# Kernel tuning notes

Measured on AMD Instinct MI355X. Metric: run time of the kernel, lower is better.

## Reference

```python
import jax, jax.numpy as jnp
import numpy as np

LEAK = 0.2

def leaky(x):
    return jnp.where(x > 0, x, LEAK * x)

def relu(x):
    return jnp.maximum(x, 0)

def conv1d(x, w):
    # x [B,Cin,L], w [Cout,Cin,3], stride 1, padding 1
    return jax.lax.conv_general_dilated(x, w, (1,), [(1, 1)],
        dimension_numbers=('NCH', 'OIH', 'NCH'))

def conv2d(x, w, pad, dil=1, groups=1):
    return jax.lax.conv_general_dilated(x, w, (1, 1), [(pad, pad), (pad, pad)],
        rhs_dilation=(dil, dil), feature_group_count=groups,
        dimension_numbers=('NCHW', 'OIHW', 'NCHW'))

def bn2d(x, p, eps=1e-5):
    # p: [4,C] = gamma, beta, running_mean, running_var (eval-mode BN)
    g, b, m, v = p
    s = (1, -1, 1, 1)
    return (x - m.reshape(s)) * (g.reshape(s) / jnp.sqrt(v.reshape(s) + eps)) + b.reshape(s)

def layernorm(x, g, b, eps=1e-5):
    mu = x.mean(-1, keepdims=True)
    var = ((x - mu) ** 2).mean(-1, keepdims=True)
    return (x - mu) / jnp.sqrt(var + eps) * g + b

def l2n(x, axis, eps):
    n = jnp.sqrt((x * x).sum(axis, keepdims=True))
    return x / jnp.maximum(n, eps)


def setup_inputs() -> dict:
    key = jax.random.key(0)
    B, C, H, W = 4, 64, 48, 48
    D, Fn, T, V = 256, 8, 4, 16
    E = 16  # orthogonal prototype embed dim
    ks = iter(jax.random.split(key, 64))
    def rn(shape, s=0.05):
        return jax.random.normal(next(ks), shape, jnp.float32) * s
    def bnp(c):
        return jnp.stack([1.0 + rn((c,), 0.1), rn((c,), 0.1), rn((c,), 0.1), 1.0 + jnp.abs(rn((c,), 0.1))])
    return dict(
        basis_vector_bank=jax.random.normal(next(ks), (T, V, D), jnp.float32),
        task_f=jax.random.normal(next(ks), (B, C, 16, 16), jnp.float32),
        img_f=jax.random.normal(next(ks), (B, C, H, W), jnp.float32),
        protos=jax.random.normal(next(ks), (T, E), jnp.float32),
        tA_w1=rn((E // 4, 1, 3)), tA_w2=rn((E // 2, E // 4, 3)),
        iA_w=rn((E // 2, C, 3, 3)), iA_bn=bnp(E // 2),
        at_w1=rn((E, Fn // 2 * E)), at_b1=rn((Fn // 2 * E,)),
        at_ln_g=jnp.ones((Fn // 2 * E,)), at_ln_b=jnp.zeros((Fn // 2 * E,)),
        at_w2=rn((Fn // 2 * E, Fn * E)), at_b2=rn((Fn * E,)),
        bv_t1=rn((D // 4, 1, 3)), bv_t2=rn((D // 2, D // 4, 3)),
        bv_ic1=rn((D // 4, C, 3, 3)), bv_bn1=bnp(D // 4),
        bv_ic2=rn((D // 2, D // 4, 3, 3)), bv_bn2=bnp(D // 2),
        bv_w1=rn((D, D // 4)), bv_b1=rn((D // 4,)),
        bv_ln_g=jnp.ones((D // 4,)), bv_ln_b=jnp.zeros((D // 4,)),
        bv_w2=rn((D // 4, D)), bv_b2=rn((D,)),
        m1_w1=rn((D, D // 4)), m1_b1=rn((D // 4,)),
        m1_ln_g=jnp.ones((D // 4,)), m1_ln_b=jnp.zeros((D // 4,)),
        m1_w2=rn((D // 4, C * C)), m1_b2=rn((C * C,)),
        m3_w1=rn((D, D // 4)), m3_b1=rn((D // 4,)),
        m3_ln_g=jnp.ones((D // 4,)), m3_ln_b=jnp.zeros((D // 4,)),
        m3_w2=rn((D // 4, 9 * C * C)), m3_b2=rn((9 * C * C,)),
        blr_bn=bnp(C),
        zc_w=rn((C, C, 1, 1), 0.01), zc_b=rn((C,), 0.01),
    )


def _forward(basis_vector_bank, task_f, img_f, protos, tA_w1, tA_w2, iA_w, iA_bn,
             at_w1, at_b1, at_ln_g, at_ln_b, at_w2, at_b2,
             bv_t1, bv_t2, bv_ic1, bv_bn1, bv_ic2, bv_bn2,
             bv_w1, bv_b1, bv_ln_g, bv_ln_b, bv_w2, bv_b2,
             m1_w1, m1_b1, m1_ln_g, m1_ln_b, m1_w2, m1_b2,
             m3_w1, m3_b1, m3_ln_g, m3_ln_b, m3_w2, m3_b2,
             blr_bn, zc_w, zc_b):
    T, V, D = basis_vector_bank.shape
    B, C, H, W = img_f.shape
    E = protos.shape[1]
    Fn = at_w2.shape[1] // E
    tau = 0.5

    # --- A2SI routing features ---
    xt = task_f.reshape(B, 1, -1)
    t1 = conv1d(leaky(conv1d(xt, tA_w1)), tA_w2).mean(-1)          # [B,E/2]
    i1 = leaky(bn2d(conv2d(img_f, iA_w, 1), iA_bn)).mean((2, 3))   # [B,E/2]
    f1 = jnp.concatenate([t1, i1], axis=1)                         # [B,E]
    h = relu(layernorm(f1 @ at_w1 + at_b1, at_ln_g, at_ln_b))
    tif = (h @ at_w2 + at_b2).reshape(B, E, Fn)                    # [B,E,F]
    logits = jnp.einsum('te,bef->bft', l2n(protos, -1, 1e-8), l2n(tif, 1, 1e-8))  # [B,F,T]

    # hard gumbel-softmax (straight-through), fixed noise key for determinism
    u = jax.random.uniform(jax.random.key(42), logits.shape, jnp.float32, 1e-10, 1.0)
    g = -jnp.log(-jnp.log(u))
    y = jax.nn.softmax((logits + g) / tau, axis=-1)
    idx = jnp.argmax(y, axis=-1)                                   # [B,F]
    y_hard = jax.nn.one_hot(idx, T, dtype=y.dtype)
    set_type = y_hard + y - jax.lax.stop_gradient(y)

    bank_flat = basis_vector_bank.reshape(T, V * D)
    sbvb = jnp.einsum('bft,tk->bfk', set_type, bank_flat).reshape(B, Fn, V, D)

    # --- BasisV_filter: filter feature ---
    xt2 = task_f.reshape(B, C, -1)
    rms = jnp.sqrt((xt2 ** 2).mean((1, 2), keepdims=True))
    xt2 = (xt2 / (rms + 1e-8)).reshape(B, 1, -1)
    te = conv1d(leaky(conv1d(xt2, bv_t1)), bv_t2).mean(-1)         # [B,D/2]
    ie = leaky(bn2d(conv2d(img_f, bv_ic1, 1), bv_bn1))
    ie = leaky(bn2d(conv2d(ie, bv_ic2, 1), bv_bn2)).mean((2, 3))   # [B,D/2]
    ff = jnp.concatenate([te, ie], axis=1)                         # [B,D]
    ff = relu(layernorm(ff @ bv_w1 + bv_b1, bv_ln_g, bv_ln_b)) @ bv_w2 + bv_b2

    # --- per-(batch,type) group gather/top-k/scatter, vectorized ---
    # group bank = bank of first filter with that type (hard one-hot -> type's bank)
    occ = idx[:, None, :] == jnp.arange(T)[None, :, None]          # [B,T,F]
    first = jnp.argmax(occ, axis=-1)                               # [B,T]
    Bg = jnp.take_along_axis(sbvb, first[:, :, None, None], axis=1)  # [B,T,V,D]
    # all rows of Q within a group are identical (filter_f expanded over F),
    # so S.max(0) == cosine(ff[b], Bg[b,t])
    scores = jnp.einsum('bd,btvd->btv', l2n(ff, -1, 1e-12), l2n(Bg, -1, 1e-12))
    order = jnp.argsort(-scores, axis=-1)                          # [B,T,V] topk order
    lt = jnp.tril(jnp.ones((Fn, Fn), bool), -1)                    # j < i
    rank = ((idx[:, :, None] == idx[:, None, :]) & lt).sum(-1)     # position in group
    bidx = jnp.arange(B)[:, None]
    sel = order[bidx, idx, rank]                                   # [B,F]
    bvf = Bg[bidx, idx, sel]                                       # [B,F,D]

    # --- per-filter dynamic convolutions ---
    w1 = relu(layernorm(bvf @ m1_w1 + m1_b1, m1_ln_g, m1_ln_b)) @ m1_w2 + m1_b2
    w1 = w1.reshape(B, Fn, C, C)                                   # [B,F,out,in]
    w3 = relu(layernorm(bvf @ m3_w1 + m3_b1, m3_ln_g, m3_ln_b)) @ m3_w2 + m3_b2
    w3 = w3.reshape(B * Fn, C, C, 3, 3)

    dp0 = jnp.einsum('bfoc,bchw->bfohw', w1, img_f)                # 1x1 branch
    xin = jnp.broadcast_to(img_f[:, None], (B, Fn, C, H, W)).reshape(1, B * Fn * C, H, W)
    ker = w3.reshape(B * Fn * C, C, 3, 3)
    dpd = [conv2d(xin, ker, d, dil=d, groups=B * Fn).reshape(B, Fn, C, H, W)
           for d in (1, 2, 3)]                                     # same-padded dilated 3x3
    t_ = idx[:, :, None, None, None]
    dp = jnp.where(t_ == 0, dp0, jnp.where(t_ == 1, dpd[0],
         jnp.where(t_ == 2, dpd[1], dpd[2])))                      # [B,F,C,H,W]

    x = leaky(bn2d(dp.reshape(B * Fn, C, H, W), blr_bn)).reshape(B, Fn, C, H, W).mean(1)
    a = conv2d(x, zc_w, 0) + zc_b.reshape(1, -1, 1, 1)
    return a + img_f


@jax.jit
def reference(basis_vector_bank, task_f, img_f, protos, tA_w1, tA_w2, iA_w, iA_bn,
              at_w1, at_b1, at_ln_g, at_ln_b, at_w2, at_b2,
              bv_t1, bv_t2, bv_ic1, bv_bn1, bv_ic2, bv_bn2,
              bv_w1, bv_b1, bv_ln_g, bv_ln_b, bv_w2, bv_b2,
              m1_w1, m1_b1, m1_ln_g, m1_ln_b, m1_w2, m1_b2,
              m3_w1, m3_b1, m3_ln_g, m3_ln_b, m3_w2, m3_b2,
              blr_bn, zc_w, zc_b):
    return _forward(basis_vector_bank, task_f, img_f, protos, tA_w1, tA_w2, iA_w, iA_bn,
                    at_w1, at_b1, at_ln_g, at_ln_b, at_w2, at_b2,
                    bv_t1, bv_t2, bv_ic1, bv_bn1, bv_ic2, bv_bn2,
                    bv_w1, bv_b1, bv_ln_g, bv_ln_b, bv_w2, bv_b2,
                    m1_w1, m1_b1, m1_ln_g, m1_ln_b, m1_w2, m1_b2,
                    m3_w1, m3_b1, m3_ln_g, m3_ln_b, m3_w2, m3_b2,
                    blr_bn, zc_w, zc_b)
```

## Files before the change

kernel.cpp:

```cpp
#include <hip/hip_runtime.h>
#include <math.h>

#define LEAKC 0.2f

#define NB 4
#define NC 64
#define LLEN 16384
#define HW 2304
#define PP 54
#define PHW 2916
#define SLABP 72
#define CP 72
#define IE1C 50

typedef __attribute__((ext_vector_type(8))) short short8;
typedef __attribute__((ext_vector_type(4))) float floatx4;

__device__ __forceinline__ float leaky(float x){ return x > 0.f ? x : LEAKC*x; }

__device__ __forceinline__ float wave_sum64(float v){
  for(int off=32;off;off>>=1) v += __shfl_xor(v,off);
  return v;
}

__device__ __forceinline__ unsigned short f2bf(float x){
  unsigned u=__float_as_uint(x);
  unsigned r=u+0x7FFFu+((u>>16)&1u);
  return (unsigned short)(r>>16);
}

__device__ __forceinline__ void threefry2x32(unsigned k0, unsigned k1, unsigned& x0, unsigned& x1){
  unsigned ks0=k0, ks1=k1, ks2=k0^k1^0x1BD11BDAu;
  x0+=ks0; x1+=ks1;
  const int rot0[4]={13,15,26,6};
  const int rot1[4]={17,29,16,24};
#define TF_APPLY(rr) {for(int r=0;r<4;r++){x0+=x1; x1=(x1<<rr[r])|(x1>>(32-rr[r])); x1^=x0;}}
  TF_APPLY(rot0); x0+=ks1; x1+=ks2+1u;
  TF_APPLY(rot1); x0+=ks2; x1+=ks0+2u;
  TF_APPLY(rot0); x0+=ks0; x1+=ks1+3u;
  TF_APPLY(rot1); x0+=ks1; x1+=ks2+4u;
  TF_APPLY(rot0); x0+=ks2; x1+=ks0+5u;
#undef TF_APPLY
}

__device__ __forceinline__ float jax_uniform128(int i){
  unsigned x0=0u, x1=(unsigned)i;
  threefry2x32(0u,42u,x0,x1);
  unsigned bits = x0 ^ x1;
  unsigned fb=(bits>>9)|0x3f800000u;
  float f=__uint_as_float(fb)-1.0f;
  float u=f*(1.0f-1e-10f)+1e-10f;
  return fmaxf(1e-10f,u);
}

struct MidSM {
  float sT[64], s0[64], sL[64];
  float red8[64][9];
  float totA_s[4]; float rms_s;
  float part[512];
  float te_s[128], t1_s[8];
  float f1[16], h[64], tif[128], tifn[128], tden[8], pden[4], pn[64], z[32];
  int sidx[8], sfirst[4], srank[8], rows[8];
  float iered[128];
  float fbuf[256], hh[64], ffn_s[256], finv_s;
  float scores[64];
  int order[64];
  float bvf[2048];
};

__global__ __launch_bounds__(256) void k_pre(const float* __restrict__ task_f,
                      const float* __restrict__ w1A, const float* __restrict__ w1B,
                      float* __restrict__ totApart, float* __restrict__ a0A, float* __restrict__ aLA,
                      float* __restrict__ totBpart, float* __restrict__ a0B, float* __restrict__ aLB,
                      float* __restrict__ rmspart,
                      const float* __restrict__ img,
                      const float* __restrict__ w1, const float* __restrict__ w2,
                      const float* __restrict__ wa,
                      unsigned short* __restrict__ imgTP,
                      unsigned short* __restrict__ W1T, unsigned short* __restrict__ W2T,
                      unsigned short* __restrict__ WAT,
                      const float* __restrict__ mw1, const float* __restrict__ mw3,
                      const float* __restrict__ bvw1p, const float* __restrict__ bvw2p,
                      const float* __restrict__ bvt2p, const float* __restrict__ atw2p,
                      const float* __restrict__ bankp,
                      const float* __restrict__ m1w2p, const float* __restrict__ m3w2p,
                      const float* __restrict__ zcwp,
                      float* __restrict__ warm, int* __restrict__ donec){
  if(blockIdx.x<256){
    int b=blockIdx.x>>6, seg=blockIdx.x&63;
    const float* x=task_f+b*LLEN;
    float tA[4]={0,0,0,0};
    float tB[64];
#pragma unroll
    for(int c=0;c<64;c++) tB[c]=0.f;
    float sq=0.f;
    int l=seg*256+threadIdx.x;
    {
      float xm=(l>0)?x[l-1]:0.f;
      float xc=x[l];
      float xp=(l<LLEN-1)?x[l+1]:0.f;
      sq=xc*xc;
#pragma unroll
      for(int c=0;c<4;c++){
        float a=leaky(w1A[c*3+0]*xm + w1A[c*3+1]*xc + w1A[c*3+2]*xp);
        tA[c]=a;
        if(l==0) a0A[b*4+c]=a;
        if(l==LLEN-1) aLA[b*4+c]=a;
      }
#pragma unroll
      for(int c=0;c<64;c++){
        float a=leaky(w1B[c*3+0]*xm + w1B[c*3+1]*xc + w1B[c*3+2]*xp);
        tB[c]=a;
        if(l==0) a0B[b*64+c]=a;
        if(l==LLEN-1) aLB[b*64+c]=a;
      }
    }
    sq=wave_sum64(sq);
#pragma unroll
    for(int c=0;c<4;c++) tA[c]=wave_sum64(tA[c]);
#pragma unroll
    for(int c=0;c<64;c++){
      float v=tB[c];
      for(int off=32;off;off>>=1) v+=__shfl_down(v,off);
      tB[c]=v;
    }
    __shared__ float redB[4][64];
    __shared__ float redA[4][4];
    __shared__ float redQ[4];
    int wave=threadIdx.x>>6, lane=threadIdx.x&63;
    if(lane==0){
#pragma unroll
      for(int c=0;c<64;c++) redB[wave][c]=tB[c];
#pragma unroll
      for(int c=0;c<4;c++) redA[wave][c]=tA[c];
      redQ[wave]=sq;
    }
    __syncthreads();
    if(threadIdx.x<64){
      float s=redB[0][threadIdx.x]+redB[1][threadIdx.x]+redB[2][threadIdx.x]+redB[3][threadIdx.x];
      totBpart[(size_t)(b*64+seg)*64+threadIdx.x]=s;
    } else if(threadIdx.x<68){
      int c=threadIdx.x-64;
      totApart[(b*64+seg)*4+c]=redA[0][c]+redA[1][c]+redA[2][c]+redA[3][c];
    } else if(threadIdx.x==68){
      rmspart[b*64+seg]=redQ[0]+redQ[1]+redQ[2]+redQ[3];
    }
  } else if(blockIdx.x<400){
    int blk=blockIdx.x-256;
    int b=blk/36, t=blk%36;
    int p0=t*64;
    __shared__ float tile[64][65];
    int pp=threadIdx.x&63, c4=threadIdx.x>>6;
    for(int r=0;r<16;r++){
      int c=c4*16+r;
      tile[c][pp]=img[(b*64+c)*HW + p0+pp];
    }
    __syncthreads();
    int pxl=threadIdx.x>>2, cg=(threadIdx.x&3)*16;
    unsigned out[8];
#pragma unroll
    for(int q=0;q<8;q++){
      unsigned lo=f2bf(tile[cg+2*q][pxl]);
      unsigned hi=f2bf(tile[cg+2*q+1][pxl]);
      out[q]=lo|(hi<<16);
    }
    int px=p0+pxl;
    int h=px/48, w=px-h*48;
    int poff=(h+3)*PP+(w+3);
    unsigned* dst=(unsigned*)(imgTP + ((size_t)(b*PHW+poff))*64 + cg);
#pragma unroll
    for(int q=0;q<8;q++) dst[q]=out[q];
  } else if(blockIdx.x<868){
    int n=(blockIdx.x-400)*256+threadIdx.x;
    if(n<9*64*64){
      int tap=n>>12, oc=(n>>6)&63, c=n&63;
      W1T[n]=f2bf(w1[oc*576+c*9+tap]);
    } else if(n<9*64*64+9*128*64){
      int m=n-9*64*64;
      int tap=m/8192, r=m-tap*8192, oc=r>>6, c=r&63;
      W2T[m]=f2bf(w2[oc*576+c*9+tap]);
    } else {
      int q=n-9*64*64-9*128*64;
      if(q<9*16*64){
        int tap=q>>10, r=q&1023, o=r>>6, c=r&63;
        WAT[q]=(o<8)?f2bf(wa[o*576+c*9+tap]):(unsigned short)0;
      }
    }
  } else if(blockIdx.x<932){
    int t=(blockIdx.x-868)*256+threadIdx.x;
    float a=0.f;
    for(int i=t;i*16<16384;i+=16384) a+=mw1[i*16];
    for(int i=t;i*16<16384;i+=16384) a+=mw3[i*16];
    for(int i=t;i*16<16384;i+=16384) a+=bvw1p[i*16];
    for(int i=t;i*16<16384;i+=16384) a+=bvw2p[i*16];
    for(int i=t;i*16<24576;i+=16384) a+=bvt2p[i*16];
    for(int i=t;i*16<8192;i+=16384) a+=atw2p[i*16];
    for(int i=t;i*16<16384;i+=16384) a+=bankp[i*16];
    for(int i=t;i*16<262144;i+=16384) a+=m1w2p[i*16];
    for(int i=t;i*16<2359296;i+=16384) a+=m3w2p[i*16];
    for(int i=t;i*16<4096;i+=16384) a+=zcwp[i*16];
    warm[t&1023]=a;
  } else {
    if(blockIdx.x==932 && threadIdx.x==0) *donec=0;
    int id=(blockIdx.x-932)*256+threadIdx.x;
    uint4 z=make_uint4(0,0,0,0);
    for(int cch=id;cch<19584;cch+=4096){
      int ck=cch&7, pxid=cch>>3;
      int b=pxid/612, p=pxid-b*612;
      int h,w;
      if(p<324){ int r=p/54; w=p-r*54; h=(r<3)?r:(r+48); }
      else { int q=p-324; int r2=q/6; int cc=q-r2*6; h=3+r2; w=(cc<3)?cc:(cc+48); }
      *(uint4*)(imgTP + ((size_t)(b*PHW + h*PP + w))*64 + ck*8)=z;
    }
  }
}

__global__ __launch_bounds__(512) void k_cm(const unsigned short* __restrict__ imgTP,
    const unsigned short* __restrict__ W1T, const unsigned short* __restrict__ W2T,
    const unsigned short* __restrict__ WAT,
    const float* __restrict__ bn1, const float* __restrict__ bn2, const float* __restrict__ bnA,
    float* __restrict__ iepart, float* __restrict__ i1part,
    const float* __restrict__ totApart, const float* __restrict__ a0A, const float* __restrict__ aLA,
    const float* __restrict__ totBpart, const float* __restrict__ a0B, const float* __restrict__ aLB,
    const float* __restrict__ rmspart,
    const float* __restrict__ tA_w2, const float* __restrict__ bv_t2,
    const float* __restrict__ at_w1, const float* __restrict__ at_b1,
    const float* __restrict__ at_ln_g, const float* __restrict__ at_ln_b,
    const float* __restrict__ at_w2, const float* __restrict__ at_b2,
    const float* __restrict__ protos,
    const float* __restrict__ bv_w1, const float* __restrict__ bv_b1,
    const float* __restrict__ bv_ln_g, const float* __restrict__ bv_ln_b,
    const float* __restrict__ bv_w2, const float* __restrict__ bv_b2,
    const float* __restrict__ bank,
    const float* __restrict__ m1_w1, const float* __restrict__ m1_b1,
    const float* __restrict__ m1_g,  const float* __restrict__ m1_bb,
    const float* __restrict__ m3_w1, const float* __restrict__ m3_b1,
    const float* __restrict__ m3_g,  const float* __restrict__ m3_bb,
    int* __restrict__ idxo, float* __restrict__ hid1, float* __restrict__ hid3,
    int* __restrict__ donec){
  __shared__ __align__(16) char smraw[75456];
  int tid=threadIdx.x;
  int lane=tid&63, wv=tid>>6;
  int n0=lane&15, kg=lane>>4;
  if(blockIdx.x<96){
    int blk=blockIdx.x;
    int b=blk/24, hp=blk-b*24;
    int h0=hp*2;
    unsigned short* slab=(unsigned short*)smraw;
    unsigned short* ie1=(unsigned short*)(smraw+46656);
    {
      const unsigned short* ibase=imgTP+((size_t)b*PHW+(size_t)(h0+1)*PP)*64;
      for(int e=tid;e<6*54*8;e+=512){
        int rr=e/(54*8), rem=e-rr*54*8, w=rem>>3, ck=rem&7;
        uint4 v=*(const uint4*)(ibase+((size_t)(rr*PP+w))*64+ck*8);
        *(uint4*)(slab+(rr*54+w)*SLABP+ck*8)=v;
      }
      if(tid<64){
        int br=tid>>4, cq=(tid>>3)&1, ck=tid&7;
        *(uint4*)(ie1+((size_t)(br*IE1C+(cq?49:0)))*CP+ck*8)=make_uint4(0,0,0,0);
      }
    }
    __syncthreads();
    {
      int mt=wv&3, rh=wv>>2;
      floatx4 acc[2][3];
#pragma unroll
      for(int rr=0;rr<2;rr++)
#pragma unroll
        for(int nt=0;nt<3;nt++) acc[rr][nt]=(floatx4){0.f,0.f,0.f,0.f};
#pragma unroll
      for(int ti=0;ti<3;ti++){
#pragma unroll
        for(int tj=0;tj<3;tj++){
          int tap=ti*3+tj;
          const unsigned short* Ab=W1T+(size_t)tap*4096;
#pragma unroll
          for(int c0=0;c0<64;c0+=32){
            short8 a=*(const short8*)(Ab+((mt*16+n0)*64+c0+kg*8));
#pragma unroll
            for(int rr=0;rr<2;rr++){
              int sr=rh*2+rr+ti;
#pragma unroll
              for(int nt=0;nt<3;nt++){
                int sc=nt*16+n0+tj+2;
                short8 bv=*(const short8*)(slab+(sr*54+sc)*SLABP+c0+kg*8);
                acc[rr][nt]=__builtin_amdgcn_mfma_f32_16x16x32_bf16(a,bv,acc[rr][nt],0,0,0);
              }
            }
          }
        }
      }
      int obase=mt*16+kg*4;
      float scale[4],m_[4],be_[4];
#pragma unroll
      for(int reg=0;reg<4;reg++){
        int o=obase+reg;
        scale[reg]=bn1[o]/sqrtf(bn1[192+o]+1e-5f);
        m_[reg]=bn1[128+o]; be_[reg]=bn1[64+o];
      }
#pragma unroll
      for(int rr=0;rr<2;rr++){
        int br=rh*2+rr;
        bool rv=((unsigned)(h0-1+br))<48u;
#pragma unroll
        for(int nt=0;nt<3;nt++){
          float v0=rv?leaky((acc[rr][nt][0]-m_[0])*scale[0]+be_[0]):0.f;
          float v1=rv?leaky((acc[rr][nt][1]-m_[1])*scale[1]+be_[1]):0.f;
          float v2=rv?leaky((acc[rr][nt][2]-m_[2])*scale[2]+be_[2]):0.f;
          float v3=rv?leaky((acc[rr][nt][3]-m_[3])*scale[3]+be_[3]):0.f;
          unsigned w0=f2bf(v0)|((unsigned)f2bf(v1)<<16);
          unsigned w1=f2bf(v2)|((unsigned)f2bf(v3)<<16);
          uint2 pk={w0,w1};
          *(uint2*)(ie1+((size_t)(br*IE1C+(nt*16+1+n0)))*CP+obase)=pk;
        }
      }
    }
    __syncthreads();
    {
      int mt2=wv;
      floatx4 acc[6];
#pragma unroll
      for(int i=0;i<6;i++) acc[i]=(floatx4){0.f,0.f,0.f,0.f};
#pragma unroll
      for(int ti=0;ti<3;ti++){
#pragma unroll
        for(int tj=0;tj<3;tj++){
          int tap=ti*3+tj;
          const unsigned short* Ab=W2T+(size_t)tap*8192;
#pragma unroll
          for(int c0=0;c0<64;c0+=32){
            short8 a=*(const short8*)(Ab+((mt2*16+n0)*64+c0+kg*8));
#pragma unroll
            for(int rr=0;rr<2;rr++){
              int sr=rr+ti;
#pragma unroll
              for(int wc=0;wc<3;wc++){
                int q=wc*16+n0+tj;
                short8 bv=*(const short8*)(ie1+((size_t)(sr*IE1C+q))*CP+c0+kg*8);
                acc[rr*3+wc]=__builtin_amdgcn_mfma_f32_16x16x32_bf16(a,bv,acc[rr*3+wc],0,0,0);
              }
            }
          }
        }
      }
      int obase=mt2*16+kg*4;
#pragma unroll
      for(int reg=0;reg<4;reg++){
        int o=obase+reg;
        float scale=bn2[o]/sqrtf(bn2[384+o]+1e-5f);
        float m_=bn2[256+o], be_=bn2[128+o];
        float part=0;
#pragma unroll
        for(int i=0;i<6;i++) part+=leaky((acc[i][reg]-m_)*scale+be_);
        for(int off=1;off<16;off<<=1) part+=__shfl_xor(part,off);
        if(n0==0) iepart[(b*24+hp)*128+o]=part*(1.f/2304.f);
      }
    }
    __syncthreads();
    if(tid==0) __hip_atomic_fetch_add(donec,1,__ATOMIC_RELEASE,__HIP_MEMORY_SCOPE_AGENT);
  } else if(blockIdx.x<108){
    int blk2=blockIdx.x-96;
    int b=blk2/3, hg=blk2%3;
    int hp=hg*8+wv;
    int h0=hp*2;
    const unsigned short* ib=imgTP+(size_t)b*PHW*64;
    floatx4 acc[6];
#pragma unroll
    for(int i=0;i<6;i++) acc[i]=(floatx4){0.f,0.f,0.f,0.f};
#pragma unroll
    for(int ti=0;ti<3;ti++){
#pragma unroll
      for(int tj=0;tj<3;tj++){
        int tap=ti*3+tj;
        const unsigned short* Ab=WAT+(size_t)tap*1024;
#pragma unroll
        for(int c0=0;c0<64;c0+=32){
          short8 a=*(const short8*)(Ab+(n0*64+c0+kg*8));
#pragma unroll
          for(int rr=0;rr<2;rr++){
            int r=h0+rr+ti-1+3;
#pragma unroll
            for(int wc=0;wc<3;wc++){
              int w=wc*16+n0+tj-1+3;
              short8 bv=*(const short8*)(ib+((size_t)(r*PP+w)*64+c0+kg*8));
              acc[rr*3+wc]=__builtin_amdgcn_mfma_f32_16x16x32_bf16(a,bv,acc[rr*3+wc],0,0,0);
            }
          }
        }
      }
    }
    int obase=kg*4;
#pragma unroll
    for(int reg=0;reg<4;reg++){
      int o=obase+reg;
      float part=0;
      if(o<8){
        float scale=bnA[o]/sqrtf(bnA[24+o]+1e-5f);
        float m_=bnA[16+o], be_=bnA[8+o];
#pragma unroll
        for(int i=0;i<6;i++) part+=leaky((acc[i][reg]-m_)*scale+be_);
      }
      for(int off=1;off<16;off<<=1) part+=__shfl_xor(part,off);
      if(n0==0 && o<8) i1part[(b*24+hp)*8+o]=part*(1.f/2304.f);
    }
    __syncthreads();
    if(tid==0) __hip_atomic_fetch_add(donec,1,__ATOMIC_RELEASE,__HIP_MEMORY_SCOPE_AGENT);
  } else {
    MidSM* S=(MidSM*)smraw;
    int b=blockIdx.x-108;
    const float invL=1.0f/16384.0f;
    {
      int c8=tid>>3, g8=tid&7;
      float s8=0;
#pragma unroll
      for(int seg=g8*8;seg<g8*8+8;seg++) s8+=totBpart[(size_t)(b*64+seg)*64+c8];
      S->red8[c8][g8]=s8;
    }
    if(tid>=64 && tid<128){
      int t=tid-64;
      S->s0[t]=a0B[b*64+t]; S->sL[t]=aLB[b*64+t];
    } else if(tid>=128 && tid<192){
      float v=rmspart[b*64+(tid-128)];
      v=wave_sum64(v);
      if(tid==128) S->rms_s=v;
    } else if(tid>=192 && tid<196){
      int c=tid-192;
      float s=0;
#pragma unroll 8
      for(int seg=0;seg<64;seg++) s+=totApart[(b*64+seg)*4+c];
      S->totA_s[c]=s;
    }
    __syncthreads();
    if(tid<64){
      float s=0;
#pragma unroll
      for(int g=0;g<8;g++) s+=S->red8[tid][g];
      S->sT[tid]=s;
    }
    __syncthreads();
    float scB=1.0f/(sqrtf(S->rms_s*invL)+1e-8f);
    if(tid<256){
      int c2=tid&127, h2=tid>>7;
      const float* wr=bv_t2+c2*192;
      float s=0;
      for(int c1=h2*32;c1<h2*32+32;c1+=8){
        float4 q[6];
        const float4* r4=(const float4*)(wr+c1*3);
#pragma unroll
        for(int u=0;u<6;u++) q[u]=r4[u];
        const float* qq=(const float*)q;
#pragma unroll
        for(int u=0;u<8;u++){
          int c=c1+u;
          float T=S->sT[c], A0=S->s0[c], AL=S->sL[c];
          s += qq[u*3+0]*(T-AL) + qq[u*3+1]*T + qq[u*3+2]*(T-A0);
        }
      }
      S->part[tid]=s;
    } else if(tid>=384 && tid<392){
      int c2=tid-384;
      float s=0;
      for(int c1=0;c1<4;c1++){
        float T=S->totA_s[c1], A0=a0A[b*4+c1], AL=aLA[b*4+c1];
        const float* w=&tA_w2[(c2*4+c1)*3];
        s += w[0]*(T-AL) + w[1]*T + w[2]*(T-A0);
      }
      S->t1_s[c2]=s*invL;
    }
    __syncthreads();
    if(tid<128) S->te_s[tid]=(S->part[tid]+S->part[tid+128])*invL*scB;
    __syncthreads();
    if(tid==0){
      while(__hip_atomic_load(donec,__ATOMIC_ACQUIRE,__HIP_MEMORY_SCOPE_AGENT)<108)
        __builtin_amdgcn_s_sleep(8);
    }
    __syncthreads();
    if(tid<8) S->f1[tid]=S->t1_s[tid];
    else if(tid<16){
      int f=tid-8;
      float s=0;
#pragma unroll
      for(int g=0;g<24;g++) s+=i1part[(b*24+g)*8+f];
      S->f1[tid]=s;
    } else if(tid>=256 && tid<384){
      int c=tid-256;
      float s=0;
#pragma unroll 8
      for(int g=0;g<24;g++) s+=iepart[(b*24+g)*128+c];
      S->iered[c]=s;
    }
    __syncthreads();
    if(tid<64){
      float s=at_b1[lane];
#pragma unroll
      for(int i=0;i<16;i++) s+=S->f1[i]*at_w1[i*64+lane];
      float mu=wave_sum64(s)*(1.f/64.f);
      float d=s-mu;
      float var=wave_sum64(d*d)*(1.f/64.f);
      S->h[lane]=fmaxf(d*(1.0f/sqrtf(var+1e-5f))*at_ln_g[lane]+at_ln_b[lane],0.f);
    }
    __syncthreads();
    if(tid<256){
      int n=tid&127, h2=tid>>7;
      float a0=0,a1=0;
      for(int k=h2*32;k<h2*32+32;k+=2){
        a0+=S->h[k]*at_w2[k*128+n];
        a1+=S->h[k+1]*at_w2[(k+1)*128+n];
      }
      S->part[tid]=a0+a1;
    }
    __syncthreads();
    if(tid<128) S->tif[tid]=at_b2[tid]+S->part[tid]+S->part[tid+128];
    __syncthreads();
    if(tid<8){
      int f=tid;
      float ss=0; for(int e=0;e<16;e++){float v=S->tif[e*8+f]; ss+=v*v;}
      S->tden[f]=fmaxf(sqrtf(ss),1e-8f);
    } else if(tid<12){
      int t=tid-8;
      float ss=0; for(int e=0;e<16;e++){float v=protos[t*16+e]; ss+=v*v;}
      S->pden[t]=fmaxf(sqrtf(ss),1e-8f);
    }
    __syncthreads();
    if(tid<128) S->tifn[tid]=S->tif[tid]/S->tden[tid&7];
    if(tid<64) S->pn[tid]=protos[tid]/S->pden[tid>>4];
    __syncthreads();
    if(tid<32){
      int f=tid>>2, t=tid&3;
      float ss=0;
#pragma unroll
      for(int e=0;e<16;e++) ss+=S->pn[t*16+e]*S->tifn[e*8+f];
      float u=jax_uniform128(b*32+f*4+t);
      float g=-logf(-logf(u));
      S->z[tid]=ss+g;
    }
    __syncthreads();
    if(tid<8){
      float best=S->z[tid*4]; int bi=0;
      for(int t=1;t<4;t++){ float v=S->z[tid*4+t]; if(v>best){best=v;bi=t;} }
      S->sidx[tid]=bi;
    }
    __syncthreads();
    if(tid<4){
      int t=tid;
      int fi=0;
      for(int f=7;f>=0;f--) if(S->sidx[f]==t) fi=f;
      S->sfirst[t]=fi;
    } else if(tid<12){
      int f=tid-4;
      int c=0; for(int f2=0;f2<f;f2++) if(S->sidx[f2]==S->sidx[f]) c++;
      S->srank[f]=c;
    }
    __syncthreads();

    if(tid<128) S->fbuf[tid]=S->te_s[tid];
    else if(tid<256) S->fbuf[tid]=S->iered[tid-128];
    __syncthreads();
    if(tid<256){
      int l64=tid&63, q=tid>>6;
      float a0=0,a1=0,a2=0,a3=0;
      for(int k=q*64;k<q*64+64;k+=4){
        a0+=S->fbuf[k]  *bv_w1[k*64+l64];
        a1+=S->fbuf[k+1]*bv_w1[(k+1)*64+l64];
        a2+=S->fbuf[k+2]*bv_w1[(k+2)*64+l64];
        a3+=S->fbuf[k+3]*bv_w1[(k+3)*64+l64];
      }
      S->part[tid]=((a0+a1)+(a2+a3));
    }
    __syncthreads();
    if(tid<64){
      float s=bv_b1[lane]+S->part[lane]+S->part[64+lane]+S->part[128+lane]+S->part[192+lane];
      float mu=wave_sum64(s)*(1.f/64.f);
      float d=s-mu;
      float var=wave_sum64(d*d)*(1.f/64.f);
      S->hh[lane]=fmaxf(d*(1.0f/sqrtf(var+1e-5f))*bv_ln_g[lane]+bv_ln_b[lane],0.f);
    }
    __syncthreads();
    {
      int n=tid&255, h2=tid>>8;
      float a0=0,a1=0;
      for(int k=h2*32;k<h2*32+32;k+=2){
        a0+=S->hh[k]*bv_w2[k*256+n];
        a1+=S->hh[k+1]*bv_w2[(k+1)*256+n];
      }
      S->part[tid]=a0+a1;
    }
    __syncthreads();
    if(tid<256) S->ffn_s[tid]=bv_b2[tid]+S->part[tid]+S->part[tid+256];
    __syncthreads();
    if(tid<64){
      float sq=0;
#pragma unroll
      for(int u=0;u<4;u++){ float v=S->ffn_s[u*64+lane]; sq+=v*v; }
      sq=wave_sum64(sq);
      if(lane==0) S->finv_s=1.0f/fmaxf(sqrtf(sq),1e-12f);
    }
    __syncthreads();
    if(tid<256) S->ffn_s[tid]*=S->finv_s;
    __syncthreads();

    if(tid<128){
      int it=tid&63, h2=tid>>6;
      int t=it>>4, v=it&15;
      int tt=S->sidx[S->sfirst[t]];
      const float4* row=(const float4*)(bank+(tt*16+v)*256);
      float sa=0,na=0;
      for(int d4=h2*32;d4<h2*32+32;d4++){
        float4 r=row[d4];
        const float* fp=&S->ffn_s[d4*4];
        sa+=fp[0]*r.x+fp[1]*r.y+fp[2]*r.z+fp[3]*r.w;
        na+=r.x*r.x+r.y*r.y+r.z*r.z+r.w*r.w;
      }
      S->part[tid]=sa;
      S->part[256+tid]=na;
    }
    __syncthreads();
    if(tid<64) S->scores[tid]=(S->part[tid]+S->part[tid+64])/fmaxf(sqrtf(S->part[256+tid]+S->part[320+tid]),1e-12f);
    __syncthreads();
    if(tid<4){
      const float* sc=&S->scores[tid*16];
      unsigned used=0;
      for(int pk=0;pk<16;pk++){
        int best=-1; float bv=-1e30f;
        for(int v2=0;v2<16;v2++){
          if(used&(1u<<v2)) continue;
          float vv=sc[v2];
          if(best<0||vv>bv){bv=vv;best=v2;}
        }
        used|=1u<<best;
        S->order[tid*16+pk]=best;
      }
    }
    __syncthreads();
    if(tid<8){
      int t=S->sidx[tid];
      int v=S->order[t*16+S->srank[tid]];
      S->rows[tid]=t*16+v;
      idxo[b*8+tid]=t;
    }
    __syncthreads();

    for(int ii=tid;ii<2048;ii+=512){
      int r=ii>>8, d=ii&255;
      S->bvf[ii]=bank[S->rows[r]*256+d];
    }
    __syncthreads();
    {
      int r=wv;
      const float* bp=&S->bvf[r*256];
      float a0=0,a1=0,a2=0,a3=0;
      float c0=0,c1=0,c2=0,c3=0;
      for(int d=0;d<256;d+=4){
        float b0=bp[d],b1=bp[d+1],b2=bp[d+2],b3=bp[d+3];
        a0+=b0*m1_w1[d*64+lane];
        a1+=b1*m1_w1[(d+1)*64+lane];
        a2+=b2*m1_w1[(d+2)*64+lane];
        a3+=b3*m1_w1[(d+3)*64+lane];
        c0+=b0*m3_w1[d*64+lane];
        c1+=b1*m3_w1[(d+1)*64+lane];
        c2+=b2*m3_w1[(d+2)*64+lane];
        c3+=b3*m3_w1[(d+3)*64+lane];
      }
      float s1=m1_b1[lane]+((a0+a1)+(a2+a3));
      float s3=m3_b1[lane]+((c0+c1)+(c2+c3));
      float mu=wave_sum64(s1)*(1.f/64.f);
      float dd=s1-mu;
      float var=wave_sum64(dd*dd)*(1.f/64.f);
      hid1[(b*8+r)*64+lane]=fmaxf(dd*(1.0f/sqrtf(var+1e-5f))*m1_g[lane]+m1_bb[lane],0.f);
      mu=wave_sum64(s3)*(1.f/64.f);
      dd=s3-mu;
      var=wave_sum64(dd*dd)*(1.f/64.f);
      hid3[(b*8+r)*64+lane]=fmaxf(dd*(1.0f/sqrtf(var+1e-5f))*m3_g[lane]+m3_bb[lane],0.f);
    }
  }
}

__global__ __launch_bounds__(256) void k_heads(const float* __restrict__ hid1, const float* __restrict__ hid3,
                        const float* __restrict__ w2a, const float* __restrict__ b2a,
                        const float* __restrict__ w2b, const float* __restrict__ b2b,
                        unsigned short* __restrict__ A1, unsigned short* __restrict__ A3){
  __shared__ float hl[2048];
  if(blockIdx.x<16){
    int n=blockIdx.x*256+threadIdx.x;
    float wcol[64];
#pragma unroll
    for(int k=0;k<64;k++) wcol[k]=w2a[k*4096+n];
    float bb=b2a[n];
    for(int i=threadIdx.x;i<2048;i+=256) hl[i]=hid1[i];
    __syncthreads();
    for(int bf=0;bf<32;bf++){
      float s=bb;
#pragma unroll
      for(int k=0;k<64;k++) s+=hl[bf*64+k]*wcol[k];
      A1[bf*4096+n]=f2bf(s);
    }
  } else {
    int n=(blockIdx.x-16)*256+threadIdx.x;
    float wcol[64];
#pragma unroll
    for(int k=0;k<64;k++) wcol[k]=w2b[(size_t)k*36864+n];
    float bb=b2b[n];
    for(int i=threadIdx.x;i<2048;i+=256) hl[i]=hid3[i];
    __syncthreads();
    int o=n/576, rem=n-o*576;
    int c=rem/9, tap=rem-c*9;
    size_t base=((size_t)tap*64+o)*64+c;
    for(int bf=0;bf<32;bf++){
      float s=bb;
#pragma unroll
      for(int k=0;k<64;k++) s+=hl[bf*64+k]*wcol[k];
      A3[(size_t)bf*9*4096+base]=f2bf(s);
    }
  }
}

__global__ __launch_bounds__(512) void k_dynF(const unsigned short* __restrict__ imgTP,
                       const unsigned short* __restrict__ A1, const unsigned short* __restrict__ A3,
                       const int* __restrict__ idx, const float* __restrict__ bn,
                       const float* __restrict__ zc_w, const float* __restrict__ zc_b,
                       const float* __restrict__ img, float* __restrict__ out){
  int blk=blockIdx.x;
  int b=blk/48, r0=blk-b*48;
  int tid=threadIdx.x;
  int lane=tid&63, w8=tid>>6;
  int mt=w8&3, fh=w8>>2;
  int n0=lane&15, kg=lane>>4;
  __shared__ unsigned short slab[7*54*SLABP];
  __shared__ float xl[64*50];
  __shared__ float zl[4096];
  int tts[4];
#pragma unroll
  for(int i=0;i<4;i++) tts[i]=idx[b*8+fh*4+i];
  int obase=mt*16+kg*4;
  float scale[4],m_[4],be_[4];
#pragma unroll
  for(int reg=0;reg<4;reg++){
    int o=obase+reg;
    scale[reg]=bn[o]/sqrtf(bn[192+o]+1e-5f);
    m_[reg]=bn[128+o]; be_[reg]=bn[64+o];
  }
  for(int i=tid;i<4096;i+=512) zl[i]=zc_w[i];
  for(int i=tid;i<3200;i+=512) xl[i]=0.f;
  {
    const unsigned short* ibase=imgTP+((size_t)b*PHW+(size_t)r0*PP)*64;
    for(int e=tid;e<7*54*8;e+=512){
      int rr=e/(54*8), rem=e-rr*54*8, w=rem>>3, ck=rem&7;
      uint4 v=*(const uint4*)(ibase + ((size_t)(rr*PP+w))*64 + ck*8);
      *(uint4*)(slab + (rr*54+w)*SLABP + ck*8)=v;
    }
  }
  __syncthreads();
  float xsum[3][4];
#pragma unroll
  for(int wc=0;wc<3;wc++)
#pragma unroll
    for(int reg=0;reg<4;reg++) xsum[wc][reg]=0.f;
#pragma unroll
  for(int fi=0;fi<4;fi++){
    int f=fh*4+fi;
    int bf=b*8+f;
    int tt=tts[fi];
    floatx4 acc[3];
#pragma unroll
    for(int i=0;i<3;i++) acc[i]=(floatx4){0.f,0.f,0.f,0.f};
    if(tt==0){
      const unsigned short* Ab=A1+(size_t)bf*4096;
#pragma unroll
      for(int c0=0;c0<64;c0+=32){
        short8 a=*(const short8*)(Ab+((mt*16+n0)*64+c0+kg*8));
#pragma unroll
        for(int wc=0;wc<3;wc++){
          short8 bv=*(const short8*)(slab + (3*54 + wc*16+n0+3)*SLABP + c0+kg*8);
          acc[wc]=__builtin_amdgcn_mfma_f32_16x16x32_bf16(a,bv,acc[wc],0,0,0);
        }
      }
    } else {
      int d=tt;
      const unsigned short* A3b=A3+(size_t)bf*9*4096;
#pragma unroll
      for(int ti=0;ti<3;ti++){
        int lr=d*(ti-1)+3;
#pragma unroll
        for(int tj=0;tj<3;tj++){
          int tap=ti*3+tj;
          int dw=d*(tj-1)+3;
          const unsigned short* Ab=A3b+(size_t)tap*4096;
#pragma unroll
          for(int c0=0;c0<64;c0+=32){
            short8 a=*(const short8*)(Ab+((mt*16+n0)*64+c0+kg*8));
#pragma unroll
            for(int wc=0;wc<3;wc++){
              short8 bv=*(const short8*)(slab + (lr*54 + wc*16+n0+dw)*SLABP + c0+kg*8);
              acc[wc]=__builtin_amdgcn_mfma_f32_16x16x32_bf16(a,bv,acc[wc],0,0,0);
            }
          }
        }
      }
    }
#pragma unroll
    for(int wc=0;wc<3;wc++)
#pragma unroll
      for(int reg=0;reg<4;reg++)
        xsum[wc][reg]+=leaky((acc[wc][reg]-m_[reg])*scale[reg]+be_[reg]);
  }
#pragma unroll
  for(int wc=0;wc<3;wc++)
#pragma unroll
    for(int reg=0;reg<4;reg++)
      atomicAdd(&xl[(obase+reg)*50 + wc*16+n0], xsum[wc][reg]*0.125f);
  __syncthreads();
  size_t base=(size_t)b*64*HW + r0*48;
  for(int e=tid;e<3072;e+=512){
    int o=e/48, px=e-o*48;
    float s=zc_b[o];
#pragma unroll
    for(int c=0;c<64;c++) s+=zl[o*64+c]*xl[c*50+px];
    size_t a=base+(size_t)o*HW+px;
    out[a]=s+img[a];
  }
}

extern "C" void kernel_launch(void* const* d_in, const int* in_sizes, int n_in,
                              void* d_out, int out_size, void* d_ws, size_t ws_size,
                              hipStream_t stream){
  const float* bank   =(const float*)d_in[0];
  const float* task_f =(const float*)d_in[1];
  const float* img_f  =(const float*)d_in[2];
  const float* protos =(const float*)d_in[3];
  const float* tA_w1  =(const float*)d_in[4];
  const float* tA_w2  =(const float*)d_in[5];
  const float* iA_w   =(const float*)d_in[6];
  const float* iA_bn  =(const float*)d_in[7];
  const float* at_w1  =(const float*)d_in[8];
  const float* at_b1  =(const float*)d_in[9];
  const float* at_ln_g=(const float*)d_in[10];
  const float* at_ln_b=(const float*)d_in[11];
  const float* at_w2  =(const float*)d_in[12];
  const float* at_b2  =(const float*)d_in[13];
  const float* bv_t1  =(const float*)d_in[14];
  const float* bv_t2  =(const float*)d_in[15];
  const float* bv_ic1 =(const float*)d_in[16];
  const float* bv_bn1 =(const float*)d_in[17];
  const float* bv_ic2 =(const float*)d_in[18];
  const float* bv_bn2 =(const float*)d_in[19];
  const float* bv_w1  =(const float*)d_in[20];
  const float* bv_b1  =(const float*)d_in[21];
  const float* bv_ln_g=(const float*)d_in[22];
  const float* bv_ln_b=(const float*)d_in[23];
  const float* bv_w2  =(const float*)d_in[24];
  const float* bv_b2  =(const float*)d_in[25];
  const float* m1_w1  =(const float*)d_in[26];
  const float* m1_b1  =(const float*)d_in[27];
  const float* m1_ln_g=(const float*)d_in[28];
  const float* m1_ln_b=(const float*)d_in[29];
  const float* m1_w2  =(const float*)d_in[30];
  const float* m1_b2  =(const float*)d_in[31];
  const float* m3_w1  =(const float*)d_in[32];
  const float* m3_b1  =(const float*)d_in[33];
  const float* m3_ln_g=(const float*)d_in[34];
  const float* m3_ln_b=(const float*)d_in[35];
  const float* m3_w2  =(const float*)d_in[36];
  const float* m3_b2  =(const float*)d_in[37];
  const float* blr_bn =(const float*)d_in[38];
  const float* zc_w   =(const float*)d_in[39];
  const float* zc_b   =(const float*)d_in[40];

  float* ws=(float*)d_ws;
  float* totApart=ws+0;
  float* a0A  =ws+1024;
  float* aLA  =ws+1040;
  float* totBpart=ws+1056;
  float* a0B  =ws+17440;
  float* aLB  =ws+17696;
  float* rmspart=ws+17952;
  float* i1part =ws+18208;
  float* iepart =ws+18976;
  int*   idxp   =(int*)(ws+31264);
  float* hid1=ws+31296;
  float* hid3=ws+33344;
  unsigned short* A1p  =(unsigned short*)(ws+35392);
  unsigned short* A3p  =(unsigned short*)(ws+100928);
  unsigned short* imgTP=(unsigned short*)(ws+690752);
  unsigned short* W1Tp =(unsigned short*)(ws+1064000);
  unsigned short* W2Tp =(unsigned short*)(ws+1082432);
  unsigned short* WATp =(unsigned short*)(ws+1119296);
  float* warm =ws+1123904;
  int*   donec=(int*)(ws+1124928);

  k_pre<<<948,256,0,stream>>>(task_f, tA_w1, bv_t1,
                              totApart, a0A, aLA, totBpart, a0B, aLB, rmspart,
                              img_f, bv_ic1, bv_ic2, iA_w, imgTP, W1Tp, W2Tp, WATp,
                              m1_w1, m3_w1, bv_w1, bv_w2, bv_t2, at_w2, bank,
                              m1_w2, m3_w2, zc_w, warm, donec);
  k_cm<<<112,512,0,stream>>>(imgTP, W1Tp, W2Tp, WATp, bv_bn1, bv_bn2, iA_bn,
                             iepart, i1part,
                             totApart, a0A, aLA, totBpart, a0B, aLB, rmspart,
                             tA_w2, bv_t2,
                             at_w1, at_b1, at_ln_g, at_ln_b, at_w2, at_b2, protos,
                             bv_w1, bv_b1, bv_ln_g, bv_ln_b, bv_w2, bv_b2, bank,
                             m1_w1, m1_b1, m1_ln_g, m1_ln_b,
                             m3_w1, m3_b1, m3_ln_g, m3_ln_b,
                             idxp, hid1, hid3, donec);
  k_heads<<<160,256,0,stream>>>(hid1, hid3, m1_w2, m1_b2, m3_w2, m3_b2, A1p, A3p);
  k_dynF<<<192,512,0,stream>>>(imgTP, A1p, A3p, idxp, blr_bn, zc_w, zc_b, img_f, (float*)d_out);

  (void)in_sizes; (void)n_in; (void)out_size; (void)ws_size;
}
```

Measured before the change: 266.1 us.

## Fuse head GEMMs and dynamic conv into one kernel with atomic-counter handoff

Merges the k_heads and k_dynF kernels into a single launch. The first 80 blocks compute the A1/A3 head weights and bump a global counter. The remaining 192 conv blocks stage their image slab, then spin until all producers are done. This removes one kernel launch and its boundary, and lets slab loading overlap with head computation. The cost is spin-waiting, and the scheme depends on all 272 blocks being co-resident. The zc weights now reuse the slab's shared memory after the MFMA phase.

```diff
diff --git a/kernel.cpp b/kernel.cpp
--- a/kernel.cpp
+++ b/kernel.cpp
@@ -61,7 +61,6 @@
   float te_s[128], t1_s[8];
   float f1[16], h[64], tif[128], tifn[128], tden[8], pden[4], pn[64], z[32];
   int sidx[8], sfirst[4], srank[8], rows[8];
-  float iered[128];
   float fbuf[256], hh[64], ffn_s[256], finv_s;
   float scores[64];
   int order[64];
@@ -85,7 +84,7 @@
                       const float* __restrict__ bankp,
                       const float* __restrict__ m1w2p, const float* __restrict__ m3w2p,
                       const float* __restrict__ zcwp,
-                      float* __restrict__ warm, int* __restrict__ donec){
+                      float* __restrict__ warm, int* __restrict__ cnt){
   if(blockIdx.x<256){
     int b=blockIdx.x>>6, seg=blockIdx.x&63;
     const float* x=task_f+b*LLEN;
@@ -201,7 +200,8 @@
     for(int i=t;i*16<4096;i+=16384) a+=zcwp[i*16];
     warm[t&1023]=a;
   } else {
-    if(blockIdx.x==932 && threadIdx.x==0) *donec=0;
+    if(blockIdx.x==932 && threadIdx.x<4)
+      __hip_atomic_store(&cnt[threadIdx.x],0,__ATOMIC_RELAXED,__HIP_MEMORY_SCOPE_AGENT);
     int id=(blockIdx.x-932)*256+threadIdx.x;
     uint4 z=make_uint4(0,0,0,0);
     for(int cch=id;cch<19584;cch+=4096){
@@ -237,7 +237,7 @@
     const float* __restrict__ m3_w1, const float* __restrict__ m3_b1,
     const float* __restrict__ m3_g,  const float* __restrict__ m3_bb,
     int* __restrict__ idxo, float* __restrict__ hid1, float* __restrict__ hid3,
-    int* __restrict__ donec){
+    int* __restrict__ cnt){
   __shared__ __align__(16) char smraw[75456];
   int tid=threadIdx.x;
   int lane=tid&63, wv=tid>>6;
@@ -357,7 +357,7 @@
       }
     }
     __syncthreads();
-    if(tid==0) __hip_atomic_fetch_add(donec,1,__ATOMIC_RELEASE,__HIP_MEMORY_SCOPE_AGENT);
+    if(tid==0) __hip_atomic_fetch_add(&cnt[0],1,__ATOMIC_RELEASE,__HIP_MEMORY_SCOPE_AGENT);
   } else if(blockIdx.x<108){
     int blk2=blockIdx.x-96;
     int b=blk2/3, hg=blk2%3;
@@ -404,7 +404,7 @@
       if(n0==0 && o<8) i1part[(b*24+hp)*8+o]=part*(1.f/2304.f);
     }
     __syncthreads();
-    if(tid==0) __hip_atomic_fetch_add(donec,1,__ATOMIC_RELEASE,__HIP_MEMORY_SCOPE_AGENT);
+    if(tid==0) __hip_atomic_fetch_add(&cnt[0],1,__ATOMIC_RELEASE,__HIP_MEMORY_SCOPE_AGENT);
   } else {
     MidSM* S=(MidSM*)smraw;
     int b=blockIdx.x-108;
@@ -471,7 +471,7 @@
     if(tid<128) S->te_s[tid]=(S->part[tid]+S->part[tid+128])*invL*scB;
     __syncthreads();
     if(tid==0){
-      while(__hip_atomic_load(donec,__ATOMIC_ACQUIRE,__HIP_MEMORY_SCOPE_AGENT)<108)
+      while(__hip_atomic_load(&cnt[0],__ATOMIC_ACQUIRE,__HIP_MEMORY_SCOPE_AGENT)<108)
         __builtin_amdgcn_s_sleep(8);
     }
     __syncthreads();
@@ -487,7 +487,7 @@
       float s=0;
 #pragma unroll 8
       for(int g=0;g<24;g++) s+=iepart[(b*24+g)*128+c];
-      S->iered[c]=s;
+      S->fbuf[128+c]=s;
     }
     __syncthreads();
     if(tid<64){
@@ -554,7 +554,6 @@
     __syncthreads();
 
     if(tid<128) S->fbuf[tid]=S->te_s[tid];
-    else if(tid<256) S->fbuf[tid]=S->iered[tid-128];
     __syncthreads();
     if(tid<256){
       int l64=tid&63, q=tid>>6;
@@ -675,148 +674,157 @@
   }
 }
 
-__global__ __launch_bounds__(256) void k_heads(const float* __restrict__ hid1, const float* __restrict__ hid3,
-                        const float* __restrict__ w2a, const float* __restrict__ b2a,
-                        const float* __restrict__ w2b, const float* __restrict__ b2b,
-                        unsigned short* __restrict__ A1, unsigned short* __restrict__ A3){
-  __shared__ float hl[2048];
-  if(blockIdx.x<16){
-    int n=blockIdx.x*256+threadIdx.x;
-    float wcol[64];
-#pragma unroll
-    for(int k=0;k<64;k++) wcol[k]=w2a[k*4096+n];
-    float bb=b2a[n];
-    for(int i=threadIdx.x;i<2048;i+=256) hl[i]=hid1[i];
-    __syncthreads();
-    for(int bf=0;bf<32;bf++){
-      float s=bb;
-#pragma unroll
-      for(int k=0;k<64;k++) s+=hl[bf*64+k]*wcol[k];
-      A1[bf*4096+n]=f2bf(s);
-    }
+__global__ __launch_bounds__(512) void k_hd(const float* __restrict__ hid1, const float* __restrict__ hid3,
+    const float* __restrict__ w2a, const float* __restrict__ b2a,
+    const float* __restrict__ w2b, const float* __restrict__ b2b,
+    unsigned short* __restrict__ A1, unsigned short* __restrict__ A3,
+    const unsigned short* __restrict__ imgTP, const int* __restrict__ idx,
+    const float* __restrict__ bn,
+    const float* __restrict__ zc_w, const float* __restrict__ zc_b,
+    const float* __restrict__ img, float* __restrict__ out,
+    int* __restrict__ cnt){
+  __shared__ __align__(16) char smraw[67232];
+  int tid=threadIdx.x;
+  if(blockIdx.x<80){
+    float* hl=(float*)smraw;
+    if(blockIdx.x<8){
+      int n=blockIdx.x*512+tid;
+      float wcol[64];
+#pragma unroll
+      for(int k=0;k<64;k++) wcol[k]=w2a[k*4096+n];
+      float bb=b2a[n];
+      for(int i=tid;i<2048;i+=512) hl[i]=hid1[i];
+      __syncthreads();
+      for(int bf=0;bf<32;bf++){
+        float s=bb;
+#pragma unroll
+        for(int k=0;k<64;k++) s+=hl[bf*64+k]*wcol[k];
+        A1[bf*4096+n]=f2bf(s);
+      }
+    } else {
+      int n=(blockIdx.x-8)*512+tid;
+      float wcol[64];
+#pragma unroll
+      for(int k=0;k<64;k++) wcol[k]=w2b[(size_t)k*36864+n];
+      float bb=b2b[n];
+      for(int i=tid;i<2048;i+=512) hl[i]=hid3[i];
+      __syncthreads();
+      int o=n/576, rem=n-o*576;
+      int c=rem/9, tap=rem-c*9;
+      size_t base=((size_t)tap*64+o)*64+c;
+      for(int bf=0;bf<32;bf++){
+        float s=bb;
+#pragma unroll
+        for(int k=0;k<64;k++) s+=hl[bf*64+k]*wcol[k];
+        A3[(size_t)bf*9*4096+base]=f2bf(s);
+      }
+    }
+    __syncthreads();
+    if(tid==0) __hip_atomic_fetch_add(&cnt[3],1,__ATOMIC_RELEASE,__HIP_MEMORY_SCOPE_AGENT);
   } else {
-    int n=(blockIdx.x-16)*256+threadIdx.x;
-    float wcol[64];
-#pragma unroll
-    for(int k=0;k<64;k++) wcol[k]=w2b[(size_t)k*36864+n];
-    float bb=b2b[n];
-    for(int i=threadIdx.x;i<2048;i+=256) hl[i]=hid3[i];
-    __syncthreads();
-    int o=n/576, rem=n-o*576;
-    int c=rem/9, tap=rem-c*9;
-    size_t base=((size_t)tap*64+o)*64+c;
-    for(int bf=0;bf<32;bf++){
-      float s=bb;
-#pragma unroll
-      for(int k=0;k<64;k++) s+=hl[bf*64+k]*wcol[k];
-      A3[(size_t)bf*9*4096+base]=f2bf(s);
-    }
-  }
-}
-
-__global__ __launch_bounds__(512) void k_dynF(const unsigned short* __restrict__ imgTP,
-                       const unsigned short* __restrict__ A1, const unsigned short* __restrict__ A3,
-                       const int* __restrict__ idx, const float* __restrict__ bn,
-                       const float* __restrict__ zc_w, const float* __restrict__ zc_b,
-                       const float* __restrict__ img, float* __restrict__ out){
-  int blk=blockIdx.x;
-  int b=blk/48, r0=blk-b*48;
-  int tid=threadIdx.x;
-  int lane=tid&63, w8=tid>>6;
-  int mt=w8&3, fh=w8>>2;
-  int n0=lane&15, kg=lane>>4;
-  __shared__ unsigned short slab[7*54*SLABP];
-  __shared__ float xl[64*50];
-  __shared__ float zl[4096];
-  int tts[4];
-#pragma unroll
-  for(int i=0;i<4;i++) tts[i]=idx[b*8+fh*4+i];
-  int obase=mt*16+kg*4;
-  float scale[4],m_[4],be_[4];
-#pragma unroll
-  for(int reg=0;reg<4;reg++){
-    int o=obase+reg;
-    scale[reg]=bn[o]/sqrtf(bn[192+o]+1e-5f);
-    m_[reg]=bn[128+o]; be_[reg]=bn[64+o];
-  }
-  for(int i=tid;i<4096;i+=512) zl[i]=zc_w[i];
-  for(int i=tid;i<3200;i+=512) xl[i]=0.f;
-  {
-    const unsigned short* ibase=imgTP+((size_t)b*PHW+(size_t)r0*PP)*64;
-    for(int e=tid;e<7*54*8;e+=512){
-      int rr=e/(54*8), rem=e-rr*54*8, w=rem>>3, ck=rem&7;
-      uint4 v=*(const uint4*)(ibase + ((size_t)(rr*PP+w))*64 + ck*8);
-      *(uint4*)(slab + (rr*54+w)*SLABP + ck*8)=v;
-    }
-  }
-  __syncthreads();
-  float xsum[3][4];
-#pragma unroll
-  for(int wc=0;wc<3;wc++)
-#pragma unroll
-    for(int reg=0;reg<4;reg++) xsum[wc][reg]=0.f;
-#pragma unroll
-  for(int fi=0;fi<4;fi++){
-    int f=fh*4+fi;
-    int bf=b*8+f;
-    int tt=tts[fi];
-    floatx4 acc[3];
-#pragma unroll
-    for(int i=0;i<3;i++) acc[i]=(floatx4){0.f,0.f,0.f,0.f};
-    if(tt==0){
-      const unsigned short* Ab=A1+(size_t)bf*4096;
-#pragma unroll
-      for(int c0=0;c0<64;c0+=32){
-        short8 a=*(const short8*)(Ab+((mt*16+n0)*64+c0+kg*8));
-#pragma unroll
-        for(int wc=0;wc<3;wc++){
-          short8 bv=*(const short8*)(slab + (3*54 + wc*16+n0+3)*SLABP + c0+kg*8);
-          acc[wc]=__builtin_amdgcn_mfma_f32_16x16x32_bf16(a,bv,acc[wc],0,0,0);
+    int dblk=blockIdx.x-80;
+    int b=dblk/48, r0=dblk-b*48;
+    int lane=tid&63, w8=tid>>6;
+    int mt=w8&3, fh=w8>>2;
+    int n0=lane&15, kg=lane>>4;
+    unsigned short* slab=(unsigned short*)smraw;
+    float* xl=(float*)(smraw+54432);
+    int tts[4];
+#pragma unroll
+    for(int i=0;i<4;i++) tts[i]=idx[b*8+fh*4+i];
+    int obase=mt*16+kg*4;
+    float scale[4],m_[4],be_[4];
+#pragma unroll
+    for(int reg=0;reg<4;reg++){
+      int o=obase+reg;
+      scale[reg]=bn[o]/sqrtf(bn[192+o]+1e-5f);
+      m_[reg]=bn[128+o]; be_[reg]=bn[64+o];
+    }
+    for(int i=tid;i<3200;i+=512) xl[i]=0.f;
+    {
+      const unsigned short* ibase=imgTP+((size_t)b*PHW+(size_t)r0*PP)*64;
+      for(int e=tid;e<7*54*8;e+=512){
+        int rr=e/(54*8), rem=e-rr*54*8, w=rem>>3, ck=rem&7;
+        uint4 v=*(const uint4*)(ibase + ((size_t)(rr*PP+w))*64 + ck*8);
+        *(uint4*)(slab + (rr*54+w)*SLABP + ck*8)=v;
+      }
+    }
+    if(tid==0){
+      while(__hip_atomic_load(&cnt[3],__ATOMIC_ACQUIRE,__HIP_MEMORY_SCOPE_AGENT)<80)
+        __builtin_amdgcn_s_sleep(8);
+    }
+    __syncthreads();
+    float xsum[3][4];
+#pragma unroll
+    for(int wc=0;wc<3;wc++)
+#pragma unroll
+      for(int reg=0;reg<4;reg++) xsum[wc][reg]=0.f;
+#pragma unroll
+    for(int fi=0;fi<4;fi++){
+      int f=fh*4+fi;
+      int bf=b*8+f;
+      int tt=tts[fi];
+      floatx4 acc[3];
+#pragma unroll
+      for(int i=0;i<3;i++) acc[i]=(floatx4){0.f,0.f,0.f,0.f};
+      if(tt==0){
+        const unsigned short* Ab=A1+(size_t)bf*4096;
+#pragma unroll
+        for(int c0=0;c0<64;c0+=32){
+          short8 a=*(const short8*)(Ab+((mt*16+n0)*64+c0+kg*8));
+#pragma unroll
+          for(int wc=0;wc<3;wc++){
+            short8 bv=*(const short8*)(slab + (3*54 + wc*16+n0+3)*SLABP + c0+kg*8);
+            acc[wc]=__builtin_amdgcn_mfma_f32_16x16x32_bf16(a,bv,acc[wc],0,0,0);
+          }
         }
-      }
-    } else {
-      int d=tt;
-      const unsigned short* A3b=A3+(size_t)bf*9*4096;
-#pragma unroll
-      for(int ti=0;ti<3;ti++){
-        int lr=d*(ti-1)+3;
-#pragma unroll
-        for(int tj=0;tj<3;tj++){
-          int tap=ti*3+tj;
-          int dw=d*(tj-1)+3;
-          const unsigned short* Ab=A3b+(size_t)tap*4096;
-#pragma unroll
-          for(int c0=0;c0<64;c0+=32){
-            short8 a=*(const short8*)(Ab+((mt*16+n0)*64+c0+kg*8));
-#pragma unroll
-            for(int wc=0;wc<3;wc++){
-              short8 bv=*(const short8*)(slab + (lr*54 + wc*16+n0+dw)*SLABP + c0+kg*8);
-              acc[wc]=__builtin_amdgcn_mfma_f32_16x16x32_bf16(a,bv,acc[wc],0,0,0);
+      } else {
+        int d=tt;
+        const unsigned short* A3b=A3+(size_t)bf*9*4096;
+#pragma unroll
+        for(int ti=0;ti<3;ti++){
+          int lr=d*(ti-1)+3;
+#pragma unroll
+          for(int tj=0;tj<3;tj++){
+            int tap=ti*3+tj;
+            int dw=d*(tj-1)+3;
+            const unsigned short* Ab=A3b+(size_t)tap*4096;
+#pragma unroll
+            for(int c0=0;c0<64;c0+=32){
+              short8 a=*(const short8*)(Ab+((mt*16+n0)*64+c0+kg*8));
+#pragma unroll
+              for(int wc=0;wc<3;wc++){
+                short8 bv=*(const short8*)(slab + (lr*54 + wc*16+n0+dw)*SLABP + c0+kg*8);
+                acc[wc]=__builtin_amdgcn_mfma_f32_16x16x32_bf16(a,bv,acc[wc],0,0,0);
+              }
             }
           }
         }
       }
+#pragma unroll
+      for(int wc=0;wc<3;wc++)
+#pragma unroll
+        for(int reg=0;reg<4;reg++)
+          xsum[wc][reg]+=leaky((acc[wc][reg]-m_[reg])*scale[reg]+be_[reg]);
     }
 #pragma unroll
     for(int wc=0;wc<3;wc++)
 #pragma unroll
       for(int reg=0;reg<4;reg++)
-        xsum[wc][reg]+=leaky((acc[wc][reg]-m_[reg])*scale[reg]+be_[reg]);
-  }
-#pragma unroll
-  for(int wc=0;wc<3;wc++)
-#pragma unroll
-    for(int reg=0;reg<4;reg++)
-      atomicAdd(&xl[(obase+reg)*50 + wc*16+n0], xsum[wc][reg]*0.125f);
-  __syncthreads();
-  size_t base=(size_t)b*64*HW + r0*48;
-  for(int e=tid;e<3072;e+=512){
-    int o=e/48, px=e-o*48;
-    float s=zc_b[o];
-#pragma unroll
-    for(int c=0;c<64;c++) s+=zl[o*64+c]*xl[c*50+px];
-    size_t a=base+(size_t)o*HW+px;
-    out[a]=s+img[a];
+        atomicAdd(&xl[(obase+reg)*50 + wc*16+n0], xsum[wc][reg]*0.125f);
+    __syncthreads();
+    float* zl=(float*)smraw;
+    for(int i=tid;i<4096;i+=512) zl[i]=zc_w[i];
+    __syncthreads();
+    size_t base=(size_t)b*64*HW + r0*48;
+    for(int e=tid;e<3072;e+=512){
+      int o=e/48, px=e-o*48;
+      float s=zc_b[o];
+#pragma unroll
+      for(int c=0;c<64;c++) s+=zl[o*64+c]*xl[c*50+px];
+      size_t a=base+(size_t)o*HW+px;
+      out[a]=s+img[a];
+    }
   }
 }
 
@@ -885,13 +893,13 @@
   unsigned short* W2Tp =(unsigned short*)(ws+1082432);
   unsigned short* WATp =(unsigned short*)(ws+1119296);
   float* warm =ws+1123904;
-  int*   donec=(int*)(ws+1124928);
+  int*   cnt  =(int*)(ws+1124928);
 
   k_pre<<<948,256,0,stream>>>(task_f, tA_w1, bv_t1,
                               totApart, a0A, aLA, totBpart, a0B, aLB, rmspart,
                               img_f, bv_ic1, bv_ic2, iA_w, imgTP, W1Tp, W2Tp, WATp,
                               m1_w1, m3_w1, bv_w1, bv_w2, bv_t2, at_w2, bank,
-                              m1_w2, m3_w2, zc_w, warm, donec);
+                              m1_w2, m3_w2, zc_w, warm, cnt);
   k_cm<<<112,512,0,stream>>>(imgTP, W1Tp, W2Tp, WATp, bv_bn1, bv_bn2, iA_bn,
                              iepart, i1part,
                              totApart, a0A, aLA, totBpart, a0B, aLB, rmspart,
@@ -900,9 +908,9 @@
                              bv_w1, bv_b1, bv_ln_g, bv_ln_b, bv_w2, bv_b2, bank,
                              m1_w1, m1_b1, m1_ln_g, m1_ln_b,
                              m3_w1, m3_b1, m3_ln_g, m3_ln_b,
-                             idxp, hid1, hid3, donec);
-  k_heads<<<160,256,0,stream>>>(hid1, hid3, m1_w2, m1_b2, m3_w2, m3_b2, A1p, A3p);
-  k_dynF<<<192,512,0,stream>>>(imgTP, A1p, A3p, idxp, blr_bn, zc_w, zc_b, img_f, (float*)d_out);
+                             idxp, hid1, hid3, cnt);
+  k_hd<<<272,512,0,stream>>>(hid1, hid3, m1_w2, m1_b2, m3_w2, m3_b2, A1p, A3p,
+                             imgTP, idxp, blr_bn, zc_w, zc_b, img_f, (float*)d_out, cnt);
 
   (void)in_sizes; (void)n_in; (void)out_size; (void)ws_size;
 }
```

After: 278.9 us. +4.8%, slower.
